# Kernel optimization log

Measured on AMD Instinct MI355X. Metric: run time of the kernel, lower is better.

## Reference

```python
import jax, jax.numpy as jnp
import numpy as np

PENALTY_MATRIX = jnp.array([[0.0, 1.0, 2.0],
                            [5.0, 0.0, 1.0],
                            [20.0, 10.0, 0.0]], dtype=jnp.float32)
CRITICAL_MISS_PENALTY = 20.0


def setup_inputs() -> dict:
    key = jax.random.key(0)
    k1, k2 = jax.random.split(key)
    B, C = 4194304, 3
    outputs = jax.random.normal(k1, (B, C), dtype=jnp.float32)
    targets = jax.random.randint(k2, (B,), 0, C, dtype=jnp.int64)
    return {"outputs": outputs, "targets": targets}


def reference(outputs, targets):
    # Cross-entropy (mean over batch, no class weights)
    logp = jax.nn.log_softmax(outputs, axis=-1)              # [B, 3]
    ce_loss = -jnp.mean(jnp.take_along_axis(logp, targets[:, None].astype(jnp.int32), axis=-1))

    pred = jnp.argmax(outputs, axis=-1)                      # [B]

    # Vectorized penalty-matrix gather replaces per-sample python loop
    safety_penalty = jnp.mean(PENALTY_MATRIX[targets, pred])

    # Critical-miss penalty (class 2)
    critical_mask = targets == 2
    n_crit = jnp.sum(critical_mask).astype(jnp.float32)
    misses = jnp.sum(critical_mask & (pred != 2)).astype(jnp.float32)
    critical_penalty = jnp.where(n_crit > 0, misses / jnp.maximum(n_crit, 1.0) * CRITICAL_MISS_PENALTY, 0.0)

    return ce_loss + 0.3 * safety_penalty + 0.5 * critical_penalty
```

## Files before the change

### kernel.cpp

```cpp
#include <hip/hip_runtime.h>


__device__ __forceinline__ float wave_reduce_f(float v) {
#pragma unroll
    for (int off = 32; off > 0; off >>= 1) v += __shfl_down(v, off, 64);
    return v;
}
__device__ __forceinline__ double wave_reduce_d(double v) {
#pragma unroll
    for (int off = 32; off > 0; off >>= 1) v += __shfl_down(v, off, 64);
    return v;
}

__device__ __forceinline__ void process_quad(const float4 a, const float4 b,
                                             const float4 c, const int4 t4,
                                             float& ce, float& pen,
                                             int& crit, int& miss) {
    const float x[12] = {a.x, a.y, a.z, a.w, b.x, b.y, b.z, b.w, c.x, c.y, c.z, c.w};
    const int   t[4]  = {t4.x, t4.y, t4.z, t4.w};
#pragma unroll
    for (int s = 0; s < 4; ++s) {
        const float x0 = x[3 * s + 0], x1 = x[3 * s + 1], x2 = x[3 * s + 2];
        const int tg = t[s];

        int pred = 0;
        float best = x0;
        if (x1 > best) { best = x1; pred = 1; }
        if (x2 > best) { best = x2; pred = 2; }

        const float e0 = __expf(x0);
        const float e1 = __expf(x1);
        const float e2 = __expf(x2);
        const float lse = __logf(e0 + e1 + e2);
        const float xt = (tg == 0) ? x0 : ((tg == 1) ? x1 : x2);
        ce += (lse - xt);

        float pv;
        if (tg == 0)      pv = (float)pred;
        else if (tg == 1) pv = (pred == 0) ? 5.0f : ((pred == 1) ? 0.0f : 1.0f);
        else              pv = (pred == 0) ? 20.0f : ((pred == 1) ? 10.0f : 0.0f);
        pen += pv;

        const int is_crit = (tg == 2);
        crit += is_crit;
        miss += is_crit & (pred != 2);
    }
}

__global__ void __launch_bounds__(1024, 8) loss_main_kernel(
    const float* __restrict__ logits, const int* __restrict__ tgt,
    int nquads, float4* __restrict__ partials) {
    float ce = 0.0f, pen = 0.0f;
    int crit = 0, miss = 0;

    const float4* lv = reinterpret_cast<const float4*>(logits);
    const int4*   tv = reinterpret_cast<const int4*>(tgt);

    const int tid      = blockIdx.x * blockDim.x + threadIdx.x;
    const int nthreads = gridDim.x * blockDim.x;

    if (nquads == 2 * nthreads) {
        const int q0 = tid, q1 = tid + nthreads;
        const float4 a0 = lv[3 * q0 + 0];
        const float4 b0 = lv[3 * q0 + 1];
        const float4 c0 = lv[3 * q0 + 2];
        const float4 a1 = lv[3 * q1 + 0];
        const float4 b1 = lv[3 * q1 + 1];
        const float4 c1 = lv[3 * q1 + 2];
        const int4   t0 = tv[q0];
        const int4   t1 = tv[q1];
        process_quad(a0, b0, c0, t0, ce, pen, crit, miss);
        process_quad(a1, b1, c1, t1, ce, pen, crit, miss);
    } else {
        for (int q = tid; q < nquads; q += nthreads) {
            const float4 a = lv[3 * q + 0];
            const float4 b = lv[3 * q + 1];
            const float4 c = lv[3 * q + 2];
            const int4   t4 = tv[q];
            process_quad(a, b, c, t4, ce, pen, crit, miss);
        }
    }

    ce = wave_reduce_f(ce);
    pen = wave_reduce_f(pen);
    float fcrit = wave_reduce_f((float)crit);
    float fmiss = wave_reduce_f((float)miss);

    __shared__ float4 s_part[16];
    const int lane = threadIdx.x & 63;
    const int wid  = threadIdx.x >> 6;
    if (lane == 0) s_part[wid] = make_float4(ce, pen, fcrit, fmiss);
    __syncthreads();
    if (threadIdx.x == 0) {
        float4 r = s_part[0];
#pragma unroll
        for (int i = 1; i < 16; ++i) {
            r.x += s_part[i].x; r.y += s_part[i].y;
            r.z += s_part[i].z; r.w += s_part[i].w;
        }
        partials[blockIdx.x] = r;
    }
}

__global__ void __launch_bounds__(256) loss_final_kernel(
    const float4* __restrict__ partials, int nblocks,
    const float* __restrict__ logits, const int* __restrict__ tgt,
    int start, int total, float* __restrict__ out) {
    double ce = 0.0, pen = 0.0, cr = 0.0, mi = 0.0;
    for (int i = threadIdx.x; i < nblocks; i += 256) {
        const float4 p = partials[i];
        ce += (double)p.x; pen += (double)p.y;
        cr += (double)p.z; mi += (double)p.w;
    }
    ce = wave_reduce_d(ce); pen = wave_reduce_d(pen);
    cr = wave_reduce_d(cr); mi = wave_reduce_d(mi);

    __shared__ double sd[4][4];
    const int lane = threadIdx.x & 63;
    const int wid  = threadIdx.x >> 6;
    if (lane == 0) { sd[wid][0] = ce; sd[wid][1] = pen; sd[wid][2] = cr; sd[wid][3] = mi; }
    __syncthreads();
    if (threadIdx.x == 0) {
#pragma unroll
        for (int i = 1; i < 4; ++i) {
            sd[0][0] += sd[i][0]; sd[0][1] += sd[i][1];
            sd[0][2] += sd[i][2]; sd[0][3] += sd[i][3];
        }
        ce = sd[0][0]; pen = sd[0][1]; cr = sd[0][2]; mi = sd[0][3];

        for (int i = start; i < total; ++i) {
            const float x0 = logits[3 * i + 0], x1 = logits[3 * i + 1], x2 = logits[3 * i + 2];
            const int tg = tgt[i];
            int pred = 0;
            float best = x0;
            if (x1 > best) { best = x1; pred = 1; }
            if (x2 > best) { best = x2; pred = 2; }
            const float e0 = __expf(x0 - best), e1 = __expf(x1 - best), e2 = __expf(x2 - best);
            const float lse = best + __logf(e0 + e1 + e2);
            const float xt = (tg == 0) ? x0 : ((tg == 1) ? x1 : x2);
            ce += (double)(lse - xt);
            float pv;
            if (tg == 0)      pv = (float)pred;
            else if (tg == 1) pv = (pred == 0) ? 5.0f : ((pred == 1) ? 0.0f : 1.0f);
            else              pv = (pred == 0) ? 20.0f : ((pred == 1) ? 10.0f : 0.0f);
            pen += (double)pv;
            cr += (double)(tg == 2);
            mi += (double)((tg == 2) && (pred != 2));
        }

        const double inv_b = 1.0 / (double)total;
        const double ce_loss = ce * inv_b;
        const double safety  = pen * inv_b;
        const double crit_pen = (cr > 0.0) ? (mi / cr * 20.0) : 0.0;
        out[0] = (float)(ce_loss + 0.3 * safety + 0.5 * crit_pen);
    }
}

extern "C" void kernel_launch(void* const* d_in, const int* in_sizes, int n_in,
                              void* d_out, int out_size, void* d_ws, size_t ws_size,
                              hipStream_t stream) {
    const float* logits = (const float*)d_in[0];
    const int*   tgt    = (const int*)d_in[1];
    const int B = in_sizes[1];

    float4* partials = (float4*)d_ws;

    const int nquads = B / 4;
    int blocks = 512;
    const int needed = (nquads + 1023) / 1024;
    if (blocks > needed) blocks = needed;
    const int maxp = (int)(ws_size / sizeof(float4));
    if (blocks > maxp) blocks = maxp;
    if (blocks < 1) blocks = 1;

    loss_main_kernel<<<blocks, 1024, 0, stream>>>(logits, tgt, nquads, partials);
    loss_final_kernel<<<1, 256, 0, stream>>>(partials, blocks, logits, tgt,
                                             nquads * 4, B, (float*)d_out);
}
```

Before: 19.53 us.

## Fuse final reduction into main kernel using per-block flags and spin-wait

Merges the two-kernel reduction into one kernel: each block publishes its partial sums with atomic stores plus a ready flag, and block 0 spins on all flags before doing the final double-precision reduction and tail handling. This removes the second kernel launch and its inter-kernel gap. It adds a hipMemsetAsync to clear the flags each call. It also relies on block 0 never stalling later blocks from being scheduled, since 512 blocks of 1024 threads must all be co-resident or progress independently. The ws_size bound check is dropped.

```diff
diff --git a/kernel.cpp b/kernel.cpp
--- a/kernel.cpp
+++ b/kernel.cpp
@@ -47,9 +47,14 @@
     }
 }
 
-__global__ void __launch_bounds__(1024, 8) loss_main_kernel(
+union PackF4 { float4 f4; unsigned long long u[2]; };
+
+__global__ void __launch_bounds__(1024, 8) loss_fused_kernel(
     const float* __restrict__ logits, const int* __restrict__ tgt,
-    int nquads, float4* __restrict__ partials) {
+    int nquads, int total,
+    unsigned long long* __restrict__ partials,
+    unsigned int* __restrict__ flags,
+    float* __restrict__ out) {
     float ce = 0.0f, pen = 0.0f;
     int crit = 0, miss = 0;
 
@@ -92,43 +97,57 @@
     if (lane == 0) s_part[wid] = make_float4(ce, pen, fcrit, fmiss);
     __syncthreads();
     if (threadIdx.x == 0) {
-        float4 r = s_part[0];
+        PackF4 r;
+        r.f4 = s_part[0];
 #pragma unroll
         for (int i = 1; i < 16; ++i) {
-            r.x += s_part[i].x; r.y += s_part[i].y;
-            r.z += s_part[i].z; r.w += s_part[i].w;
+            r.f4.x += s_part[i].x; r.f4.y += s_part[i].y;
+            r.f4.z += s_part[i].z; r.f4.w += s_part[i].w;
         }
-        partials[blockIdx.x] = r;
+        __hip_atomic_store(&partials[2 * blockIdx.x + 0], r.u[0],
+                           __ATOMIC_RELAXED, __HIP_MEMORY_SCOPE_AGENT);
+        __hip_atomic_store(&partials[2 * blockIdx.x + 1], r.u[1],
+                           __ATOMIC_RELAXED, __HIP_MEMORY_SCOPE_AGENT);
+        asm volatile("s_waitcnt vmcnt(0)" ::: "memory");
+        __hip_atomic_store(&flags[blockIdx.x], 1u,
+                           __ATOMIC_RELAXED, __HIP_MEMORY_SCOPE_AGENT);
     }
-}
 
-__global__ void __launch_bounds__(256) loss_final_kernel(
-    const float4* __restrict__ partials, int nblocks,
-    const float* __restrict__ logits, const int* __restrict__ tgt,
-    int start, int total, float* __restrict__ out) {
-    double ce = 0.0, pen = 0.0, cr = 0.0, mi = 0.0;
-    for (int i = threadIdx.x; i < nblocks; i += 256) {
-        const float4 p = partials[i];
-        ce += (double)p.x; pen += (double)p.y;
-        cr += (double)p.z; mi += (double)p.w;
+    if (blockIdx.x != 0) return;
+
+    const int nb = (int)gridDim.x;
+    if ((int)threadIdx.x < nb) {
+        while (__hip_atomic_load(&flags[threadIdx.x],
+                                 __ATOMIC_RELAXED, __HIP_MEMORY_SCOPE_AGENT) == 0u) {
+        }
     }
-    ce = wave_reduce_d(ce); pen = wave_reduce_d(pen);
-    cr = wave_reduce_d(cr); mi = wave_reduce_d(mi);
+    __syncthreads();
 
-    __shared__ double sd[4][4];
-    const int lane = threadIdx.x & 63;
-    const int wid  = threadIdx.x >> 6;
-    if (lane == 0) { sd[wid][0] = ce; sd[wid][1] = pen; sd[wid][2] = cr; sd[wid][3] = mi; }
+    double dce = 0.0, dpen = 0.0, dcr = 0.0, dmi = 0.0;
+    if ((int)threadIdx.x < nb) {
+        PackF4 p;
+        p.u[0] = __hip_atomic_load(&partials[2 * threadIdx.x + 0],
+                                   __ATOMIC_RELAXED, __HIP_MEMORY_SCOPE_AGENT);
+        p.u[1] = __hip_atomic_load(&partials[2 * threadIdx.x + 1],
+                                   __ATOMIC_RELAXED, __HIP_MEMORY_SCOPE_AGENT);
+        dce = (double)p.f4.x; dpen = (double)p.f4.y;
+        dcr = (double)p.f4.z; dmi = (double)p.f4.w;
+    }
+    dce = wave_reduce_d(dce); dpen = wave_reduce_d(dpen);
+    dcr = wave_reduce_d(dcr); dmi = wave_reduce_d(dmi);
+
+    __shared__ double sd[16][4];
+    if (lane == 0) { sd[wid][0] = dce; sd[wid][1] = dpen; sd[wid][2] = dcr; sd[wid][3] = dmi; }
     __syncthreads();
     if (threadIdx.x == 0) {
 #pragma unroll
-        for (int i = 1; i < 4; ++i) {
+        for (int i = 1; i < 16; ++i) {
             sd[0][0] += sd[i][0]; sd[0][1] += sd[i][1];
             sd[0][2] += sd[i][2]; sd[0][3] += sd[i][3];
         }
-        ce = sd[0][0]; pen = sd[0][1]; cr = sd[0][2]; mi = sd[0][3];
+        dce = sd[0][0]; dpen = sd[0][1]; dcr = sd[0][2]; dmi = sd[0][3];
 
-        for (int i = start; i < total; ++i) {
+        for (int i = nquads * 4; i < total; ++i) {
             const float x0 = logits[3 * i + 0], x1 = logits[3 * i + 1], x2 = logits[3 * i + 2];
             const int tg = tgt[i];
             int pred = 0;
@@ -138,20 +157,20 @@
             const float e0 = __expf(x0 - best), e1 = __expf(x1 - best), e2 = __expf(x2 - best);
             const float lse = best + __logf(e0 + e1 + e2);
             const float xt = (tg == 0) ? x0 : ((tg == 1) ? x1 : x2);
-            ce += (double)(lse - xt);
+            dce += (double)(lse - xt);
             float pv;
             if (tg == 0)      pv = (float)pred;
             else if (tg == 1) pv = (pred == 0) ? 5.0f : ((pred == 1) ? 0.0f : 1.0f);
             else              pv = (pred == 0) ? 20.0f : ((pred == 1) ? 10.0f : 0.0f);
-            pen += (double)pv;
-            cr += (double)(tg == 2);
-            mi += (double)((tg == 2) && (pred != 2));
+            dpen += (double)pv;
+            dcr += (double)(tg == 2);
+            dmi += (double)((tg == 2) && (pred != 2));
         }
 
         const double inv_b = 1.0 / (double)total;
-        const double ce_loss = ce * inv_b;
-        const double safety  = pen * inv_b;
-        const double crit_pen = (cr > 0.0) ? (mi / cr * 20.0) : 0.0;
+        const double ce_loss = dce * inv_b;
+        const double safety  = dpen * inv_b;
+        const double crit_pen = (dcr > 0.0) ? (dmi / dcr * 20.0) : 0.0;
         out[0] = (float)(ce_loss + 0.3 * safety + 0.5 * crit_pen);
     }
 }
@@ -163,17 +182,17 @@
     const int*   tgt    = (const int*)d_in[1];
     const int B = in_sizes[1];
 
-    float4* partials = (float4*)d_ws;
+    unsigned long long* partials = (unsigned long long*)d_ws;
+    unsigned int*       flags    = (unsigned int*)((char*)d_ws + 8192);
 
     const int nquads = B / 4;
     int blocks = 512;
     const int needed = (nquads + 1023) / 1024;
     if (blocks > needed) blocks = needed;
-    const int maxp = (int)(ws_size / sizeof(float4));
-    if (blocks > maxp) blocks = maxp;
     if (blocks < 1) blocks = 1;
 
-    loss_main_kernel<<<blocks, 1024, 0, stream>>>(logits, tgt, nquads, partials);
-    loss_final_kernel<<<1, 256, 0, stream>>>(partials, blocks, logits, tgt,
-                                             nquads * 4, B, (float*)d_out);
+    hipMemsetAsync(flags, 0, (size_t)blocks * sizeof(unsigned int), stream);
+
+    loss_fused_kernel<<<blocks, 1024, 0, stream>>>(logits, tgt, nquads, B,
+                                                   partials, flags, (float*)d_out);
 }
```

New measurement: 25.34 us. 1.3x slower.
